# Performance work log

Hardware: AMD Instinct MI355X
Metric: run time of the kernel (lower is better)

## Reference

```python
import jax, jax.numpy as jnp
import numpy as np

MEAN_DEG = 3.8
QS = (2, 4, 8, 16, 32, 64)
POOL_DIM = 100
BP_ITERS = 10


def _bn(x, g, b):
    # BatchNorm1d in training mode: biased batch statistics over the node dim
    m = x.mean(0)
    v = ((x - m) ** 2).mean(0)
    return g * (x - m) * jax.lax.rsqrt(v + 1e-5) + b


def _gcn_sparse(x, src, dst, n, w, b):
    # GCNConv: add self loops, symmetric deg^-1/2 normalization, scatter-add aggregation
    loop = jnp.arange(n, dtype=src.dtype)
    s2 = jnp.concatenate([src, loop])
    d2 = jnp.concatenate([dst, loop])
    deg = jax.ops.segment_sum(jnp.ones(s2.shape[0], x.dtype), d2, num_segments=n)
    dinv = jnp.where(deg > 0, jax.lax.rsqrt(deg), 0.0)
    norm = (dinv[s2] * dinv[d2])[:, None]
    return jax.ops.segment_sum((x @ w)[s2] * norm, d2, num_segments=n) + b


def _gcn_dense(x, adj, w, b):
    # GCN on the dense pooled adjacency (pooled graphs are fully connected)
    n = adj.shape[-1]
    A = adj + jnp.eye(n, dtype=adj.dtype)
    d = A.sum(-1)
    dinv = jnp.where(d > 0, jax.lax.rsqrt(d), 0.0)
    An = dinv[:, :, None] * A * dinv[:, None, :]
    return jnp.einsum('bij,bjd->bid', An, x @ w) + b


def _bp(src, dst, n, q, beta, seed):
    # SBM-style belief propagation: iterate node marginals psi [n,q] for a fixed
    # number of sweeps; coupling exp(beta), global external field ~ mean_degree.
    key = jax.random.fold_in(jax.random.key(42), seed)
    psi0 = jax.nn.softmax(jax.random.normal(key, (n, q), jnp.float32), -1)
    eb = jnp.expm1(beta)

    def step(psi, _):
        msg = jax.ops.segment_sum(jnp.log1p(eb * psi[src]), dst, num_segments=n)
        field = (MEAN_DEG * beta / n) * psi.sum(0)
        return jax.nn.softmax(msg - field, -1), None

    psi, _ = jax.lax.scan(step, psi0, None, length=BP_ITERS)
    return psi


def _forward(x, w11, b11, g11, be11, w12, b12, g12, be12, w13, b13, g13, be13,
             bp_betas, pool_w, pool_b,
             w21, b21, g21, be21, w22, b22, g22, be22, w23, b23, g23, be23,
             fc1_w, fc1_b, fc2_w, fc2_b, edge_index, num_graphs):
    n = x.shape[0]
    B = num_graphs
    N = n // B
    src, dst = edge_index[0], edge_index[1]
    # per-graph dense adjacency (edge_index_to_csr -> todense, duplicates sum)
    adj = jnp.zeros((B, N, N), x.dtype).at[src // N, src % N, dst % N].add(1.0)

    # stage 1: three GCN + BN layers on the raw graph
    x11 = _bn(_gcn_sparse(x, src, dst, n, w11, b11), g11, be11)
    x12 = _bn(_gcn_sparse(x11, src, dst, n, w12, b12), g12, be12)
    x13 = _bn(_gcn_sparse(x12, src, dst, n, w13, b13), g13, be13)
    x1_out = jnp.concatenate([x11, x12, x13], -1).reshape(B, N, -1).max(1)  # [B,90]

    # six belief-propagation runs -> concat assignments [n, 2+4+...+64 = 126]
    s1 = jnp.concatenate([_bp(src, dst, n, q, bp_betas[i], i) for i, q in enumerate(QS)], -1)
    s1 = s1 @ pool_w + pool_b  # [n, 100]

    # dense diff-pool
    s1 = jax.nn.softmax(s1.reshape(B, N, POOL_DIM), -1)
    p1_x = jnp.einsum('bnk,bnd->bkd', s1, x13.reshape(B, N, -1))   # [B,100,30]
    p1_adj = jnp.einsum('bnk,bnm,bml->bkl', s1, adj, s1)           # [B,100,100]

    # stage 2: three dense GCN + BN layers on pooled graphs
    C = 30
    x21 = _bn(_gcn_dense(p1_x, p1_adj, w21, b21).reshape(-1, C), g21, be21)
    x22 = _bn(_gcn_dense(x21.reshape(B, POOL_DIM, C), p1_adj, w22, b22).reshape(-1, C), g22, be22)
    x23 = _bn(_gcn_dense(x22.reshape(B, POOL_DIM, C), p1_adj, w23, b23).reshape(-1, C), g23, be23)
    x2_out = jnp.concatenate([x21, x22, x23], -1).reshape(B, POOL_DIM, -1).max(1)  # [B,90]

    conv_out = jnp.concatenate([x1_out, x2_out], -1)  # [B,180]
    out = jax.nn.relu(conv_out @ fc1_w + fc1_b) @ fc2_w + fc2_b  # dropout p=0 -> identity
    return out, jnp.zeros((1,), x.dtype)


def setup_inputs() -> dict:
    key = jax.random.key(0)
    B, N, EP = 64, 1024, 8192
    ks = jax.random.split(key, 24)
    x = jax.random.normal(ks[0], (B * N, 3), jnp.float32)
    off = (jnp.arange(B, dtype=jnp.int32) * N)[:, None]
    src = (jax.random.randint(ks[1], (B, EP), 0, N, jnp.int32) + off).reshape(-1)
    dst = (jax.random.randint(ks[2], (B, EP), 0, N, jnp.int32) + off).reshape(-1)
    edge_index = jnp.stack([src, dst])

    def lin(k, i, o):
        return jax.random.normal(k, (i, o), jnp.float32) / np.sqrt(i)

    p = {}
    dims1 = [(3, 30), (30, 30), (30, 30)]
    for idx, (i, o) in enumerate(dims1, 1):
        p['w1%d' % idx] = lin(ks[2 + idx], i, o)
        p['b1%d' % idx] = jnp.zeros((o,), jnp.float32)
        p['g1%d' % idx] = jnp.ones((o,), jnp.float32)
        p['be1%d' % idx] = jnp.zeros((o,), jnp.float32)
    for idx in (1, 2, 3):
        p['w2%d' % idx] = lin(ks[8 + idx], 30, 30)
        p['b2%d' % idx] = jnp.zeros((30,), jnp.float32)
        p['g2%d' % idx] = jnp.ones((30,), jnp.float32)
        p['be2%d' % idx] = jnp.zeros((30,), jnp.float32)
    qs = np.array(QS, np.float32)
    p['bp_betas'] = jnp.asarray(np.log(qs / (np.sqrt(MEAN_DEG) - 1.0) + 1.0))
    p['pool_w'] = lin(ks[15], 126, 100); p['pool_b'] = jnp.zeros((100,), jnp.float32)
    p['fc1_w'] = lin(ks[16], 180, 50); p['fc1_b'] = jnp.zeros((50,), jnp.float32)
    p['fc2_w'] = lin(ks[17], 50, 6); p['fc2_b'] = jnp.zeros((6,), jnp.float32)
    return {'x': x, 'edge_index': edge_index, 'num_graphs': B, **p}


def reference(x, edge_index, num_graphs, w11, b11, g11, be11, w12, b12, g12, be12,
              w13, b13, g13, be13, bp_betas, pool_w, pool_b,
              w21, b21, g21, be21, w22, b22, g22, be22, w23, b23, g23, be23,
              fc1_w, fc1_b, fc2_w, fc2_b):
    return _forward(x, w11, b11, g11, be11, w12, b12, g12, be12, w13, b13, g13, be13,
                    bp_betas, pool_w, pool_b,
                    w21, b21, g21, be21, w22, b22, g22, be22, w23, b23, g23, be23,
                    fc1_w, fc1_b, fc2_w, fc2_b, edge_index, num_graphs)
```

## Files before the change

### kernel.cpp

```cpp
#include <hip/hip_runtime.h>
#include <stdint.h>
#include <float.h>


constexpr int NN    = 65536;
constexpr int NEDGE = 524288;
constexpr int NBG   = 64;

__constant__ int cQS[6]   = {2,4,8,16,32,64};

__device__ __forceinline__ void tf2x32(uint32_t k0, uint32_t k1, uint32_t x0, uint32_t x1,
                                       uint32_t& o0, uint32_t& o1){
  uint32_t ks[3] = {k0, k1, k0 ^ k1 ^ 0x1BD11BDAu};
  x0 += ks[0]; x1 += ks[1];
  const int RA[4] = {13,15,26,6}, RB[4] = {17,29,16,24};
  #pragma unroll
  for (int i=0;i<5;i++){
    const int* r = (i&1)? RB : RA;
    #pragma unroll
    for (int j=0;j<4;j++){
      x0 += x1;
      x1 = (x1 << r[j]) | (x1 >> (32 - r[j]));
      x1 ^= x0;
    }
    x0 += ks[(i+1)%3];
    x1 += ks[(i+2)%3] + (uint32_t)(i+1);
  }
  o0 = x0; o1 = x1;
}

__device__ __forceinline__ float erfinv32(float xx){
  #pragma clang fp contract(off)
  float w = -log1pf(-xx*xx);
  float p;
  if (w < 5.0f){
    w = w - 2.5f;
    p = 2.81022636e-08f;
    p = 3.43273939e-07f  + p*w;
    p = -3.5233877e-06f  + p*w;
    p = -4.39150654e-06f + p*w;
    p = 0.00021858087f   + p*w;
    p = -0.00125372503f  + p*w;
    p = -0.00417768164f  + p*w;
    p = 0.246640727f     + p*w;
    p = 1.50140941f      + p*w;
  } else {
    w = sqrtf(w) - 3.0f;
    p = -0.000200214257f;
    p = 0.000100950558f  + p*w;
    p = 0.00134934322f   + p*w;
    p = -0.00367342844f  + p*w;
    p = 0.00573950773f   + p*w;
    p = -0.0076224613f   + p*w;
    p = 0.00943887047f   + p*w;
    p = 1.00167406f      + p*w;
    p = 2.83297682f      + p*w;
  }
  return p*xx;
}

__global__ __launch_bounds__(256) void k_count(const int* __restrict__ src, const int* __restrict__ dst,
                                               int* __restrict__ degi, int* __restrict__ dego){
  int e = blockIdx.x*256 + threadIdx.x;
  if (e >= NEDGE) return;
  atomicAdd(&degi[dst[e]], 1);
  atomicAdd(&dego[src[e]], 1);
}

__global__ __launch_bounds__(256) void k_scan1(const int* __restrict__ degi, const int* __restrict__ dego,
                                               int* __restrict__ rpi, int* __restrict__ rpo,
                                               int* __restrict__ bsum){
  __shared__ int lds[256];
  const int* deg = blockIdx.y? dego : degi;
  int* rp = blockIdx.y? rpo : rpi;
  int* bs = bsum + blockIdx.y*256;
  int b = blockIdx.x, t = threadIdx.x;
  lds[t] = deg[b*256 + t];
  __syncthreads();
  for (int s=1;s<256;s<<=1){
    int add = (t>=s)? lds[t-s] : 0;
    __syncthreads();
    lds[t] += add;
    __syncthreads();
  }
  rp[b*256 + t + 1] = lds[t];
  if (t==0 && b==0) rp[0] = 0;
  if (t==255) bs[b] = lds[255];
}

__global__ __launch_bounds__(256) void k_scan2(int* __restrict__ bsum){
  __shared__ int lds[256];
  int* bs = bsum + blockIdx.x*256;
  int t = threadIdx.x;
  lds[t] = bs[t];
  __syncthreads();
  for (int s=1;s<256;s<<=1){
    int add = (t>=s)? lds[t-s] : 0;
    __syncthreads();
    lds[t] += add;
    __syncthreads();
  }
  bs[t] = (t==0)? 0 : lds[t-1];
}

__global__ __launch_bounds__(256) void k_scan3(int* __restrict__ rpi, int* __restrict__ rpo,
                                               const int* __restrict__ bsum){
  int* rp = blockIdx.y? rpo : rpi;
  const int* bs = bsum + blockIdx.y*256;
  int b = blockIdx.x, t = threadIdx.x;
  rp[b*256 + t + 1] += bs[b];
}

__global__ __launch_bounds__(256) void k_fill(const int* __restrict__ src, const int* __restrict__ dst,
                                              const int* __restrict__ rpi, const int* __restrict__ rpo,
                                              int* __restrict__ cntA, int* __restrict__ cntB,
                                              int* __restrict__ colI, int* __restrict__ colO){
  int e = blockIdx.x*256 + threadIdx.x;
  if (e >= NEDGE) return;
  if (blockIdx.y == 0){
    int d = dst[e];
    int p = atomicAdd(&cntA[d], 1);
    colI[rpi[d] + p] = e;
  } else {
    int d = src[e];
    int p = atomicAdd(&cntB[d], 1);
    colO[rpo[d] + p] = e;
  }
}

__global__ __launch_bounds__(256) void k_sortrow(const int* __restrict__ rpi, const int* __restrict__ rpo,
                                                 int* __restrict__ colI, int* __restrict__ colO,
                                                 const int* __restrict__ src, const int* __restrict__ dst){
  const int* rp = blockIdx.y? rpo : rpi;
  int* colbuf   = blockIdx.y? colO : colI;
  const int* other = blockIdx.y? dst : src;
  int v = blockIdx.x*256 + threadIdx.x;
  if (v >= NN) return;
  int s0 = rp[v], s1 = rp[v+1];
  for (int i=s0+1;i<s1;i++){
    int key = colbuf[i]; int j = i-1;
    while (j>=s0 && colbuf[j]>key){ colbuf[j+1]=colbuf[j]; j--; }
    colbuf[j+1] = key;
  }
  for (int i=s0;i<s1;i++) colbuf[i] = other[colbuf[i]];
}

__global__ __launch_bounds__(256) void k_dinv(const int* __restrict__ degi, float* __restrict__ dinv){
  int v = blockIdx.x*256 + threadIdx.x;
  if (v >= NN) return;
  dinv[v] = 1.0f / sqrtf((float)(degi[v] + 1));
}

template<int CIN>
__global__ __launch_bounds__(256) void k_mm30(const float* __restrict__ x, const float* __restrict__ w,
                                              float* __restrict__ h, int nrow){
  __shared__ float ws[CIN*30];
  int t = threadIdx.x;
  for (int i=t;i<CIN*30;i+=256) ws[i] = w[i];
  __syncthreads();
  int id = blockIdx.x*256 + t;
  if (id >= nrow*30) return;
  int v = id/30, j = id - v*30;
  const float* xr = x + v*CIN;
  float acc = 0.f;
  #pragma unroll
  for (int k=0;k<CIN;k++) acc += xr[k]*ws[k*30+j];
  h[id] = acc;
}

__global__ __launch_bounds__(256) void k_gcn_agg(const float* __restrict__ h, const int* __restrict__ rp,
    const int* __restrict__ col, const float* __restrict__ dinv, const float* __restrict__ bias,
    float* __restrict__ y){
  int b = blockIdx.x;
  int xcd = b & 7, i = b >> 3;
  int gs = i/60, j = i - gs*60;
  int graph = gs*8 + xcd;
  int idwg = j*256 + threadIdx.x;
  int rw = idwg/15, pr = idwg - rw*15;
  int v = graph*1024 + rw;
  float dv = dinv[v];
  float accx = 0.f, accy = 0.f;
  int a = rp[v], e = rp[v+1];
  for (; a+4<=e; a+=4){
    int s0=col[a], s1=col[a+1], s2=col[a+2], s3=col[a+3];
    float d0=dinv[s0], d1=dinv[s1], d2=dinv[s2], d3=dinv[s3];
    float2 h0=*(const float2*)(h+s0*30+2*pr), h1=*(const float2*)(h+s1*30+2*pr);
    float2 h2=*(const float2*)(h+s2*30+2*pr), h3=*(const float2*)(h+s3*30+2*pr);
    accx += h0.x*(d0*dv); accy += h0.y*(d0*dv);
    accx += h1.x*(d1*dv); accy += h1.y*(d1*dv);
    accx += h2.x*(d2*dv); accy += h2.y*(d2*dv);
    accx += h3.x*(d3*dv); accy += h3.y*(d3*dv);
  }
  for (; a<e; ++a){
    int s = col[a];
    float w = dinv[s]*dv;
    float2 hv = *(const float2*)(h+s*30+2*pr);
    accx += hv.x*w; accy += hv.y*w;
  }
  float2 hs = *(const float2*)(h + v*30 + 2*pr);
  float w2 = dv*dv;
  accx += hs.x*w2; accy += hs.y*w2;
  float2 o; o.x = accx + bias[2*pr]; o.y = accy + bias[2*pr+1];
  *(float2*)(y + v*30 + 2*pr) = o;
}

__global__ __launch_bounds__(256) void k_bn_stat(const float* __restrict__ x, int nrow,
    float* __restrict__ partS, float* __restrict__ partQ){
  __shared__ float lds[256*31];
  int b = blockIdx.x, t = threadIdx.x;
  int rows = nrow >> 8;
  float as[30], aq[30];
  #pragma unroll
  for (int f=0;f<30;f++){ as[f]=0.f; aq[f]=0.f; }
  for (int r=t; r<rows; r+=256){
    const float* xr = x + (b*rows + r)*30;
    #pragma unroll
    for (int f=0;f<30;f++){ float v = xr[f]; as[f] += v; aq[f] += v*v; }
  }
  #pragma unroll
  for (int f=0;f<30;f++) lds[t*31+f] = as[f];
  __syncthreads();
  for (int s=128;s>0;s>>=1){
    if (t<s){
      #pragma unroll
      for (int f=0;f<30;f++) lds[t*31+f] += lds[(t+s)*31+f];
    }
    __syncthreads();
  }
  if (t<30) partS[b*30+t] = lds[t];
  __syncthreads();
  #pragma unroll
  for (int f=0;f<30;f++) lds[t*31+f] = aq[f];
  __syncthreads();
  for (int s=128;s>0;s>>=1){
    if (t<s){
      #pragma unroll
      for (int f=0;f<30;f++) lds[t*31+f] += lds[(t+s)*31+f];
    }
    __syncthreads();
  }
  if (t<30) partQ[b*30+t] = lds[t];
}

__global__ void k_bn_red2(const float* __restrict__ partS, const float* __restrict__ partQ,
                          float n, float* __restrict__ mean, float* __restrict__ var){
  int f = threadIdx.x;
  if (f >= 30) return;
  float s = 0.f, q = 0.f;
  for (int b=0;b<256;b++){ s += partS[b*30+f]; q += partQ[b*30+f]; }
  float m = s / n;
  mean[f] = m;
  var[f]  = q / n - m*m;
}

__global__ __launch_bounds__(256) void k_bn_apply(const float* __restrict__ x, const float* __restrict__ mean,
    const float* __restrict__ var, const float* __restrict__ g, const float* __restrict__ be,
    float* __restrict__ out, int nrow){
  int id = blockIdx.x*256 + threadIdx.x;
  if (id >= nrow*30) return;
  int f = id % 30;
  out[id] = g[f]*(x[id]-mean[f]) * (1.0f/sqrtf(var[f]+1e-5f)) + be[f];
}

__device__ __forceinline__ void bp_decode2(int b, int& graph, int& run, int& jj){
  int xcd = b & 7, i = b >> 3;
  int gs = i >> 7, j = i & 127;
  if      (j <   4){ run=0; jj=j;    }
  else if (j <   8){ run=1; jj=j-4;  }
  else if (j <  16){ run=2; jj=j-8;  }
  else if (j <  32){ run=3; jj=j-16; }
  else if (j <  64){ run=4; jj=j-32; }
  else             { run=5; jj=j-64; }
  graph = gs*8 + xcd;
}

template<int TPR>
__device__ __forceinline__ void bfly_max4(float& m0, float& m1, float& m2, float& m3){
  if constexpr (TPR > 1){
    #pragma unroll
    for (int lm = TPR>>1; lm; lm >>= 1){
      float p0=__shfl_xor(m0,lm,64), p1=__shfl_xor(m1,lm,64);
      float p2=__shfl_xor(m2,lm,64), p3=__shfl_xor(m3,lm,64);
      m0=fmaxf(m0,p0); m1=fmaxf(m1,p1); m2=fmaxf(m2,p2); m3=fmaxf(m3,p3);
    }
  }
  { float t0=fmaxf(m0,m2), t1=fmaxf(m1,m3), t2=fmaxf(m2,m0), t3=fmaxf(m3,m1);
    m0=t0; m1=t1; m2=t2; m3=t3; }
  { float t0=fmaxf(m0,m1), t1=fmaxf(m1,m0), t2=fmaxf(m2,m3), t3=fmaxf(m3,m2);
    m0=t0; m1=t1; m2=t2; m3=t3; }
}

template<int TPR>
__device__ __forceinline__ void bfly_sum4(float& s0, float& s1, float& s2, float& s3){
  if constexpr (TPR > 1){
    #pragma unroll
    for (int lm = TPR>>1; lm; lm >>= 1){
      float p0=__shfl_xor(s0,lm,64), p1=__shfl_xor(s1,lm,64);
      float p2=__shfl_xor(s2,lm,64), p3=__shfl_xor(s3,lm,64);
      s0 += p0; s1 += p1; s2 += p2; s3 += p3;
    }
  }
  { float t0=s0+s2, t1=s1+s3, t2=s2+s0, t3=s3+s1;
    s0=t0; s1=t1; s2=t2; s3=t3; }
  { float t0=s0+s1, t1=s1+s0, t2=s2+s3, t3=s3+s2;
    s0=t0; s1=t1; s2=t2; s3=t3; }
}

template<int Q, int CO, int TPR, int L2T>
__device__ __forceinline__ void bp_first_elem2(int graph, int jj, float* __restrict__ psi_pk,
                                               float* __restrict__ lg, float eb,
                                               uint32_t k0, uint32_t k1){
  int idx = jj*256 + (int)threadIdx.x;
  if constexpr (Q == 2){
    int row = graph*1024 + idx;
    float z[2];
    #pragma unroll
    for (int r=0;r<2;r++){
      uint32_t b0,b1;
      tf2x32(k0,k1, 0u, (uint32_t)(row*2 + r), b0,b1);
      uint32_t bits = b0 ^ b1;
      float f = __uint_as_float((bits>>9) | 0x3F800000u) - 1.0f;
      const float lo = __uint_as_float(0xBF7FFFFFu);
      float u = fmaxf(lo, f*2.0f + lo);
      z[r] = __uint_as_float(0x3FB504F3u) * erfinv32(u);
    }
    float m0=fmaxf(z[0],z[1]), m1=fmaxf(z[1],z[0]);
    float e0=expf(z[0]-m0), e1=expf(z[1]-m1);
    float s0=e0+e1, s1=e1+e0;
    float p0=e0/s0, p1=e1/s1;
    ((float2*)(psi_pk + (size_t)NN*CO))[row] = make_float2(p0,p1);
    ((float2*)(lg     + (size_t)NN*CO))[row] = make_float2(log1pf(eb*p0), log1pf(eb*p1));
  } else {
    int rw = idx >> L2T, ct = idx & (TPR-1);
    int row = graph*1024 + rw;
    float z[4];
    #pragma unroll
    for (int r=0;r<4;r++){
      uint32_t b0,b1;
      tf2x32(k0,k1, 0u, (uint32_t)(row*Q + 4*ct + r), b0,b1);
      uint32_t bits = b0 ^ b1;
      float f = __uint_as_float((bits>>9) | 0x3F800000u) - 1.0f;
      const float lo = __uint_as_float(0xBF7FFFFFu);
      float u = fmaxf(lo, f*2.0f + lo);
      z[r] = __uint_as_float(0x3FB504F3u) * erfinv32(u);
    }
    float m0=z[0],m1=z[1],m2=z[2],m3=z[3];
    bfly_max4<TPR>(m0,m1,m2,m3);
    float e0=expf(z[0]-m0), e1=expf(z[1]-m1), e2=expf(z[2]-m2), e3=expf(z[3]-m3);
    float s0=e0,s1=e1,s2=e2,s3=e3;
    bfly_sum4<TPR>(s0,s1,s2,s3);
    float p0=e0/s0, p1=e1/s1, p2=e2/s2, p3=e3/s3;
    ((float4*)(psi_pk + (size_t)NN*CO))[(size_t)row*TPR + ct] = make_float4(p0,p1,p2,p3);
    ((float4*)(lg     + (size_t)NN*CO))[(size_t)row*TPR + ct] =
        make_float4(log1pf(eb*p0), log1pf(eb*p1), log1pf(eb*p2), log1pf(eb*p3));
  }
}

__global__ __launch_bounds__(256) void k_bp_first(float* __restrict__ psi_pk, float* __restrict__ lg,
                                                  const float* __restrict__ betas){
  int graph, run, jj;
  bp_decode2(blockIdx.x, graph, run, jj);
  uint32_t k0, k1;
  tf2x32(0u, 42u, 0u, (uint32_t)run, k0, k1);
  float eb = expm1f(betas[run]);
  switch(run){
    case 0: bp_first_elem2< 2, 0, 1,0>(graph, jj, psi_pk, lg, eb, k0, k1); break;
    case 1: bp_first_elem2< 4, 2, 1,0>(graph, jj, psi_pk, lg, eb, k0, k1); break;
    case 2: bp_first_elem2< 8, 6, 2,1>(graph, jj, psi_pk, lg, eb, k0, k1); break;
    case 3: bp_first_elem2<16,14, 4,2>(graph, jj, psi_pk, lg, eb, k0, k1); break;
    case 4: bp_first_elem2<32,30, 8,3>(graph, jj, psi_pk, lg, eb, k0, k1); break;
    default:bp_first_elem2<64,62,16,4>(graph, jj, psi_pk, lg, eb, k0, k1); break;
  }
}

template<int Q, int CO, int TPR, int L2T>
__device__ __forceinline__ void bp_step_elem2(int graph, int run, int jj,
    const float* __restrict__ lcur, float* __restrict__ nxt, float* __restrict__ lnxt,
    const int* __restrict__ rp, const int* __restrict__ col,
    const float* __restrict__ field, float eb, int fin){
  int idx = jj*256 + (int)threadIdx.x;
  if constexpr (Q == 2){
    int row = graph*1024 + idx;
    const float2* B2 = (const float2*)(lcur + (size_t)NN*CO);
    float a0=0.f, a1=0.f;
    int a = rp[row], b2 = rp[row+1];
    for (; a+8<=b2; a+=8){
      int s0=col[a],s1=col[a+1],s2=col[a+2],s3=col[a+3];
      int s4=col[a+4],s5=col[a+5],s6=col[a+6],s7=col[a+7];
      float2 u0=B2[s0], u1=B2[s1], u2=B2[s2], u3=B2[s3];
      float2 u4=B2[s4], u5=B2[s5], u6=B2[s6], u7=B2[s7];
      a0+=u0.x; a1+=u0.y; a0+=u1.x; a1+=u1.y;
      a0+=u2.x; a1+=u2.y; a0+=u3.x; a1+=u3.y;
      a0+=u4.x; a1+=u4.y; a0+=u5.x; a1+=u5.y;
      a0+=u6.x; a1+=u6.y; a0+=u7.x; a1+=u7.y;
    }
    for (; a+4<=b2; a+=4){
      int s0=col[a],s1=col[a+1],s2=col[a+2],s3=col[a+3];
      float2 u0=B2[s0], u1=B2[s1], u2=B2[s2], u3=B2[s3];
      a0+=u0.x; a1+=u0.y; a0+=u1.x; a1+=u1.y;
      a0+=u2.x; a1+=u2.y; a0+=u3.x; a1+=u3.y;
    }
    for (; a<b2; ++a){ float2 u=B2[col[a]]; a0+=u.x; a1+=u.y; }
    float v0 = a0 - field[run*64 + 0];
    float v1 = a1 - field[run*64 + 1];
    float m0=fmaxf(v0,v1), m1=fmaxf(v1,v0);
    float e0=expf(v0-m0), e1=expf(v1-m1);
    float s0=e0+e1, s1=e1+e0;
    float p0=e0/s0, p1=e1/s1;
    if (fin){
      float* o = nxt + (size_t)row*126 + CO;
      o[0]=p0; o[1]=p1;
    } else {
      ((float2*)(nxt  + (size_t)NN*CO))[row] = make_float2(p0,p1);
      ((float2*)(lnxt + (size_t)NN*CO))[row] = make_float2(log1pf(eb*p0), log1pf(eb*p1));
// ... 114 lines not shown

__global__ __launch_bounds__(256) void k_catT(const float* __restrict__ cat, float* __restrict__ catT){
  __shared__ float tile[64*127];
  int b = blockIdx.x, t = threadIdx.x;
  const float* src = cat + (size_t)b*64*126;
  for (int i=t;i<8064;i+=256){
    int r = i/126, k = i - r*126;
    tile[r*127 + k] = src[i];
  }
  __syncthreads();
  for (int i=t;i<8064;i+=256){
    int k = i>>6, r = i&63;
    catT[(size_t)k*65536 + b*64 + r] = tile[r*127 + k];
  }
}

__global__ __launch_bounds__(256) void k_s1t(const float* __restrict__ catT, const float* __restrict__ pw,
                                             const float* __restrict__ pb, float* __restrict__ s1){
  __shared__ float wl[12600];
  __shared__ float pbl[100];
  __shared__ float redM[2][128];
  __shared__ float redS[2][128];
  int t = threadIdx.x;
  for (int i=t;i<12600;i+=256) wl[i] = pw[i];
  if (t < 100) pbl[t] = pb[t];
  int w = t>>6, lane = t&63;
  int rh = w&1, chh = w>>1;
  int ch = chh*50;
  int row = blockIdx.x*128 + rh*64 + lane;
  __syncthreads();
  float acc[50];
  #pragma unroll
  for (int j=0;j<50;j++) acc[j] = pbl[ch+j];
  for (int k=0;k<126;k++){
    float xv = catT[(size_t)k*65536 + row];
    const float* wr = &wl[k*100 + ch];
    #pragma unroll
    for (int j=0;j<50;j+=2){
      float2 wv = *(const float2*)&wr[j];
      acc[j]   += xv*wv.x;
      acc[j+1] += xv*wv.y;
    }
  }
  float m = acc[0];
  #pragma unroll
  for (int j=1;j<50;j++) m = fmaxf(m, acc[j]);
  redM[chh][rh*64 + lane] = m;
  __syncthreads();
  float mm = fmaxf(redM[0][rh*64 + lane], redM[1][rh*64 + lane]);
  float s = 0.f;
  #pragma unroll
  for (int j=0;j<50;j++){ acc[j] = expf(acc[j]-mm); s += acc[j]; }
  redS[chh][rh*64 + lane] = s;
  __syncthreads();
  float tot = redS[0][rh*64 + lane] + redS[1][rh*64 + lane];
  float* o = s1 + (size_t)row*100 + ch;
  #pragma unroll
  for (int j=0;j<50;j+=2){
    float2 ov; ov.x = acc[j]/tot; ov.y = acc[j+1]/tot;
    *(float2*)&o[j] = ov;
  }
}

__global__ __launch_bounds__(256) void k_T(const float* __restrict__ s1, const int* __restrict__ rp,
                                           const int* __restrict__ col, float* __restrict__ T){
  int b = blockIdx.x;
  int xcd = b & 7, i = b >> 3;
  int gs = i/100, j = i - gs*100;
  int graph = gs*8 + xcd;
  int idwg = j*256 + threadIdx.x;
  int rw = idwg/25, quad = idwg - rw*25;
  int v = graph*1024 + rw;
  float a0=0.f,a1=0.f,a2=0.f,a3=0.f;
  const float4* S4 = (const float4*)s1;
  int a = rp[v], e = rp[v+1];
  for (; a+8<=e; a+=8){
    int s0=col[a], s1_=col[a+1], s2=col[a+2], s3=col[a+3];
    int s4=col[a+4], s5=col[a+5], s6=col[a+6], s7=col[a+7];
    float4 u0=S4[(size_t)s0*25+quad], u1=S4[(size_t)s1_*25+quad];
    float4 u2=S4[(size_t)s2*25+quad], u3=S4[(size_t)s3*25+quad];
    float4 u4=S4[(size_t)s4*25+quad], u5=S4[(size_t)s5*25+quad];
    float4 u6=S4[(size_t)s6*25+quad], u7=S4[(size_t)s7*25+quad];
    a0+=u0.x; a1+=u0.y; a2+=u0.z; a3+=u0.w;
    a0+=u1.x; a1+=u1.y; a2+=u1.z; a3+=u1.w;
    a0+=u2.x; a1+=u2.y; a2+=u2.z; a3+=u2.w;
    a0+=u3.x; a1+=u3.y; a2+=u3.z; a3+=u3.w;
    a0+=u4.x; a1+=u4.y; a2+=u4.z; a3+=u4.w;
    a0+=u5.x; a1+=u5.y; a2+=u5.z; a3+=u5.w;
    a0+=u6.x; a1+=u6.y; a2+=u6.z; a3+=u6.w;
    a0+=u7.x; a1+=u7.y; a2+=u7.z; a3+=u7.w;
  }
  for (; a+4<=e; a+=4){
    int s0=col[a], s1_=col[a+1], s2=col[a+2], s3=col[a+3];
    float4 u0=S4[(size_t)s0*25+quad], u1=S4[(size_t)s1_*25+quad];
    float4 u2=S4[(size_t)s2*25+quad], u3=S4[(size_t)s3*25+quad];
    a0+=u0.x; a1+=u0.y; a2+=u0.z; a3+=u0.w;
    a0+=u1.x; a1+=u1.y; a2+=u1.z; a3+=u1.w;
    a0+=u2.x; a1+=u2.y; a2+=u2.z; a3+=u2.w;
    a0+=u3.x; a1+=u3.y; a2+=u3.z; a3+=u3.w;
  }
  for (; a<e; ++a){
    float4 u = S4[(size_t)col[a]*25+quad];
    a0+=u.x; a1+=u.y; a2+=u.z; a3+=u.w;
  }
  ((float4*)T)[(size_t)v*25 + quad] = make_float4(a0,a1,a2,a3);
}

__global__ __launch_bounds__(512) void k_p1adj_sk(const float* __restrict__ s1, const float* __restrict__ T,
                                                  float* __restrict__ part){
  __shared__ float sS[6400];
  __shared__ float sT[6400];
  int blk = blockIdx.x;
  int b = blk >> 2, qtr = blk & 3;
  int t = threadIdx.x;
  int tk = t/20, tl = t - tk*20;
  bool act = t < 500;
  int k0 = tk*4, l0 = tl*5;
  float acc[4][5];
  #pragma unroll
  for (int i=0;i<4;i++)
    #pragma unroll
    for (int j=0;j<5;j++) acc[i][j] = 0.f;
  const float* s1b = s1 + (size_t)b*102400;
  const float* Tb  = T  + (size_t)b*102400;
  for (int c=qtr*4; c<qtr*4+4; c++){
    for (int i=t;i<6400;i+=512){ sS[i] = s1b[c*6400+i]; sT[i] = Tb[c*6400+i]; }
    __syncthreads();
    if (act){
      #pragma unroll 2
      for (int n=0;n<64;n++){
        const float* sr = &sS[n*100 + k0];
        const float* tr = &sT[n*100 + l0];
        float s0=sr[0], s1v=sr[1], s2=sr[2], s3=sr[3];
        float t0=tr[0], t1=tr[1], t2=tr[2], t3=tr[3], t4=tr[4];
        acc[0][0]+=s0*t0; acc[0][1]+=s0*t1; acc[0][2]+=s0*t2; acc[0][3]+=s0*t3; acc[0][4]+=s0*t4;
        acc[1][0]+=s1v*t0; acc[1][1]+=s1v*t1; acc[1][2]+=s1v*t2; acc[1][3]+=s1v*t3; acc[1][4]+=s1v*t4;
        acc[2][0]+=s2*t0; acc[2][1]+=s2*t1; acc[2][2]+=s2*t2; acc[2][3]+=s2*t3; acc[2][4]+=s2*t4;
        acc[3][0]+=s3*t0; acc[3][1]+=s3*t1; acc[3][2]+=s3*t2; acc[3][3]+=s3*t3; acc[3][4]+=s3*t4;
      }
    }
    __syncthreads();
  }
  if (act){
    float* pp = part + (size_t)qtr*640000 + (size_t)b*10000;
    #pragma unroll
    for (int i=0;i<4;i++){
      float* o = pp + (k0+i)*100 + l0;
      #pragma unroll
      for (int j=0;j<5;j++) o[j] = acc[i][j];
    }
  }
}

__global__ __launch_bounds__(256) void k_p1adj_red(const float* __restrict__ part, float* __restrict__ padj){
  int id = blockIdx.x*256 + threadIdx.x;
  if (id >= NBG*10000) return;
  float s = part[id];
  s += part[640000 + id];
  s += part[1280000 + id];
  s += part[1920000 + id];
  padj[id] = s;
}

__global__ __launch_bounds__(256) void k_p1x_sk(const float* __restrict__ s1, const float* __restrict__ x13,
                                                float* __restrict__ part){
  __shared__ float sS[6400];
  __shared__ float sX[1920];
  int blk = blockIdx.x;
  int b = blk >> 2, qtr = blk & 3;
  int t = threadIdx.x;
  int tk = t/10, tl = t - tk*10;
  bool act = t < 250;
  int k0 = tk*4, d0 = tl*3;
  float acc[4][3];
  #pragma unroll
  for (int i=0;i<4;i++)
    #pragma unroll
    for (int j=0;j<3;j++) acc[i][j] = 0.f;
  const float* s1b = s1 + (size_t)b*102400;
  const float* xb  = x13 + (size_t)b*30720;
  for (int c=qtr*4; c<qtr*4+4; c++){
    for (int i=t;i<6400;i+=256) sS[i] = s1b[c*6400+i];
    for (int i=t;i<1920;i+=256) sX[i] = xb[c*1920+i];
    __syncthreads();
    if (act){
      #pragma unroll 2
      for (int n=0;n<64;n++){
        const float* sr = &sS[n*100 + k0];
        const float* xr = &sX[n*30 + d0];
        float s0=sr[0], s1v=sr[1], s2=sr[2], s3=sr[3];
        float x0=xr[0], x1=xr[1], x2=xr[2];
        acc[0][0]+=s0*x0; acc[0][1]+=s0*x1; acc[0][2]+=s0*x2;
        acc[1][0]+=s1v*x0; acc[1][1]+=s1v*x1; acc[1][2]+=s1v*x2;
        acc[2][0]+=s2*x0; acc[2][1]+=s2*x1; acc[2][2]+=s2*x2;
        acc[3][0]+=s3*x0; acc[3][1]+=s3*x1; acc[3][2]+=s3*x2;
      }
    }
    __syncthreads();
  }
  if (act){
    float* pp = part + (size_t)qtr*192000 + (size_t)b*3000;
    #pragma unroll
    for (int i=0;i<4;i++){
      float* o = pp + (k0+i)*30 + d0;
      #pragma unroll
      for (int j=0;j<3;j++) o[j] = acc[i][j];
    }
  }
}

__global__ __launch_bounds__(256) void k_p1x_red(const float* __restrict__ part, float* __restrict__ px){
  int id = blockIdx.x*256 + threadIdx.x;
  if (id >= NBG*3000) return;
  float s = part[id];
  s += part[192000 + id];
  s += part[384000 + id];
  s += part[576000 + id];
  px[id] = s;
}

__global__ __launch_bounds__(256) void k_dinv2(const float* __restrict__ padj, float* __restrict__ dv){
  int id = blockIdx.x*256 + threadIdx.x;
  if (id >= NBG*100) return;
  const float* r = padj + id*100;
  int k = id % 100;
  float s = 0.f;
  for (int l=0;l<100;l++){
    float v = r[l];
    if (l==k) v += 1.0f;
    s += v;
  }
  dv[id] = 1.0f/sqrtf(s);
}

__global__ __launch_bounds__(256) void k_Ank(const float* __restrict__ padj, const float* __restrict__ dv,
                                             float* __restrict__ An){
  int id = blockIdx.x*256 + threadIdx.x;
  if (id >= NBG*10000) return;
  int b = id/10000;
  int rem = id - b*10000;
  int k = rem/100, l = rem - k*100;
  float a = padj[id] + ((k==l)? 1.0f : 0.0f);
  An[id] = (dv[b*100+k]*a)*dv[b*100+l];
}

__global__ __launch_bounds__(256) void k_y2(const float* __restrict__ An, const float* __restrict__ h,
    const float* __restrict__ bias, float* __restrict__ y){
  int id = blockIdx.x*256 + threadIdx.x;
  if (id >= NBG*100*30) return;
  int d = id % 30;
  int bk = id / 30;
  int b = bk / 100;
  const float* Ar = An + bk*100;
  const float* hb = h + b*100*30;
  float acc = 0.f;
  for (int l=0;l<100;l++) acc += Ar[l]*hb[l*30+d];
  y[id] = acc + bias[d];
}

__global__ __launch_bounds__(256) void k_pool2(const float* __restrict__ A,
    const float* __restrict__ Bv, const float* __restrict__ Cv,
    int rows, float* __restrict__ conv, int coff){
  __shared__ float lds[256*31];
  int b = blockIdx.x, a = blockIdx.y, t = threadIdx.x;
  const float* X = (a==0)? A : ((a==1)? Bv : Cv);
  float acc[30];
  #pragma unroll
  for (int f=0;f<30;f++) acc[f] = -FLT_MAX;
  for (int r=t; r<rows; r+=256){
    const float* xr = X + (size_t)(b*rows + r)*30;
    #pragma unroll
    for (int f=0;f<30;f++) acc[f] = fmaxf(acc[f], xr[f]);
  }
  #pragma unroll
  for (int f=0;f<30;f++) lds[t*31+f] = acc[f];
  __syncthreads();
  for (int s=128;s>0;s>>=1){
    if (t<s){
      #pragma unroll
      for (int f=0;f<30;f++) lds[t*31+f] = fmaxf(lds[t*31+f], lds[(t+s)*31+f]);
    }
    __syncthreads();
  }
  if (t<30) conv[b*180 + coff + a*30 + t] = lds[t];
}

__global__ __launch_bounds__(64) void k_fc(const float* __restrict__ conv,
    const float* __restrict__ w1, const float* __restrict__ b1,
    const float* __restrict__ w2, const float* __restrict__ b2, float* __restrict__ out){
  __shared__ float row[180];
  __shared__ float hid[50];
  int b = blockIdx.x, t = threadIdx.x;
  for (int i=t;i<180;i+=64) row[i] = conv[b*180+i];
  __syncthreads();
  if (t < 50){
    float a = b1[t];
    for (int i=0;i<180;i++) a += row[i]*w1[i*50+t];
    hid[t] = fmaxf(a, 0.f);
  }
  __syncthreads();
  if (t < 6){
    float a = b2[t];
    for (int i=0;i<50;i++) a += hid[i]*w2[i*6+t];
    out[b*6+t] = a;
  }
  if (b==0 && t==63) out[NBG*6] = 0.0f;
}

extern "C" void kernel_launch(void* const* d_in, const int* in_sizes, int n_in,
                              void* d_out, int out_size, void* d_ws, size_t ws_size,
                              hipStream_t stream)
{
  (void)in_sizes; (void)n_in; (void)out_size; (void)ws_size;
  const float* x   = (const float*)d_in[0];
  const int*   src = (const int*)d_in[1];
  const int*   dst = src + NEDGE;
  const float* w11=(const float*)d_in[3],  *b11=(const float*)d_in[4],  *g11=(const float*)d_in[5],  *be11=(const float*)d_in[6];
  const float* w12=(const float*)d_in[7],  *b12=(const float*)d_in[8],  *g12=(const float*)d_in[9],  *be12=(const float*)d_in[10];
  const float* w13=(const float*)d_in[11], *b13=(const float*)d_in[12], *g13=(const float*)d_in[13], *be13=(const float*)d_in[14];
  const float* w21=(const float*)d_in[15], *b21=(const float*)d_in[16], *g21=(const float*)d_in[17], *be21=(const float*)d_in[18];
  const float* w22=(const float*)d_in[19], *b22=(const float*)d_in[20], *g22=(const float*)d_in[21], *be22=(const float*)d_in[22];
  const float* w23=(const float*)d_in[23], *b23=(const float*)d_in[24], *g23=(const float*)d_in[25], *be23=(const float*)d_in[26];
  const float* betas=(const float*)d_in[27];
  const float* poolw=(const float*)d_in[28], *poolb=(const float*)d_in[29];
  const float* fc1w=(const float*)d_in[30], *fc1b=(const float*)d_in[31];
  const float* fc2w=(const float*)d_in[32], *fc2b=(const float*)d_in[33];
  float* out = (float*)d_out;

  uint8_t* basep = (uint8_t*)d_ws;
  size_t off = 0;
  auto take = [&](size_t bytes)->void*{
    void* p = basep + off;
    off = (off + bytes + 255) & ~(size_t)255;
    return p;
  };
  int* degi    = (int*)take((size_t)NN*4);
  int* dego    = (int*)take((size_t)NN*4);
  int* cntA    = (int*)take((size_t)NN*4);
  int* cntB    = (int*)take((size_t)NN*4);
  int* rp_in   = (int*)take((size_t)(NN+1)*4);
  int* rp_out  = (int*)take((size_t)(NN+1)*4);
  int* bsum    = (int*)take(512*4);
  int* col_in  = (int*)take((size_t)NEDGE*4);
  int* col_out = (int*)take((size_t)NEDGE*4);
  float* dinv  = (float*)take((size_t)NN*4);
  float* hbuf  = (float*)take((size_t)NN*30*4);
  float* tmpY  = (float*)take((size_t)NN*30*4);
  float* X1    = (float*)take((size_t)NN*30*4);
  float* X2    = (float*)take((size_t)NN*30*4);
  float* X3    = (float*)take((size_t)NN*30*4);
  float* bufA  = (float*)take((size_t)NN*126*4);
  float* bufB  = (float*)take((size_t)NN*126*4);
  float* logA  = (float*)take((size_t)NN*126*4);
  float* logB  = (float*)take((size_t)NN*126*4);
  float* partCS= (float*)take((size_t)6*256*64*4);
  float* fieldv= (float*)take(384*4);
  float* partBN= (float*)take(256*30*4);
  float* partBN2=(float*)take(256*30*4);
  float* meanv = (float*)take(128);
  float* varv  = (float*)take(128);
  float* px    = (float*)take(192000*4);
  float* padj  = (float*)take(640000*4);
  float* An    = (float*)take(640000*4);
  float* dinv2 = (float*)take(6400*4);
  float* h2    = (float*)take(192000*4);
  float* y2    = (float*)take(192000*4);
  float* X21   = (float*)take(192000*4);
  float* X22   = (float*)take(192000*4);
  float* X23   = (float*)take(192000*4);
  float* conv  = (float*)take(64*180*4);

  float* catT     = logA;
  float* pAdjPart = logB;
  float* pPxPart  = logB + 2560000;

  hipMemsetAsync(degi, 0, (size_t)4*NN*4, stream);
  k_count<<<2048,256,0,stream>>>(src,dst,degi,dego);
  k_scan1<<<dim3(256,2),256,0,stream>>>(degi, dego, rp_in, rp_out, bsum);
  k_scan2<<<2,256,0,stream>>>(bsum);
  k_scan3<<<dim3(256,2),256,0,stream>>>(rp_in, rp_out, bsum);
  k_fill<<<dim3(2048,2),256,0,stream>>>(src, dst, rp_in, rp_out, cntA, cntB, col_in, col_out);
  k_sortrow<<<dim3(256,2),256,0,stream>>>(rp_in, rp_out, col_in, col_out, src, dst);
  k_dinv<<<256,256,0,stream>>>(degi, dinv);

  auto run_bn = [&](const float* yin, float* xout, const float* g, const float* be, int nrow){
    k_bn_stat<<<256,256,0,stream>>>(yin, nrow, partBN, partBN2);
    k_bn_red2<<<1,32,0,stream>>>(partBN, partBN2, (float)nrow, meanv, varv);
    k_bn_apply<<<(nrow*30)/256,256,0,stream>>>(yin, meanv, varv, g, be, xout, nrow);
  };

  k_mm30<3><<<7680,256,0,stream>>>(x, w11, hbuf, NN);
  k_gcn_agg<<<3840,256,0,stream>>>(hbuf, rp_in, col_in, dinv, b11, tmpY);
  run_bn(tmpY, X1, g11, be11, NN);
  k_mm30<30><<<7680,256,0,stream>>>(X1, w12, hbuf, NN);
  k_gcn_agg<<<3840,256,0,stream>>>(hbuf, rp_in, col_in, dinv, b12, tmpY);
  run_bn(tmpY, X2, g12, be12, NN);
  k_mm30<30><<<7680,256,0,stream>>>(X2, w13, hbuf, NN);
  k_gcn_agg<<<3840,256,0,stream>>>(hbuf, rp_in, col_in, dinv, b13, tmpY);
  run_bn(tmpY, X3, g13, be13, NN);
  k_pool2<<<dim3(NBG,3),256,0,stream>>>(X1, X2, X3, 1024, conv, 0);

  k_bp_first<<<8192,256,0,stream>>>(bufA, logA, betas);
  float* cur = bufA;  float* nxt = bufB;
  float* lcur = logA; float* lnxt = logB;
  for (int it=0; it<10; ++it){
    k_colsum_part<<<1536,64,0,stream>>>(cur, partCS);
    k_field<<<1,384,0,stream>>>(partCS, betas, fieldv);
    int fin = (it==9);
    k_bp_step<<<8192,256,0,stream>>>(nxt, lcur, lnxt, rp_in, col_in, fieldv, betas, fin);
    float* tp = cur;  cur = nxt;   nxt = tp;
    float* tl = lcur; lcur = lnxt; lnxt = tl;
  }

  k_catT<<<1024,256,0,stream>>>(bufA, catT);
  k_s1t<<<512,256,0,stream>>>(catT, poolw, poolb, bufB);
  k_T<<<6400,256,0,stream>>>(bufB, rp_out, col_out, bufA);
  k_p1adj_sk<<<256,512,0,stream>>>(bufB, bufA, pAdjPart);
  k_p1adj_red<<<2500,256,0,stream>>>(pAdjPart, padj);
  k_p1x_sk<<<256,256,0,stream>>>(bufB, X3, pPxPart);
  k_p1x_red<<<750,256,0,stream>>>(pPxPart, px);
  k_dinv2<<<25,256,0,stream>>>(padj, dinv2);
  k_Ank<<<2500,256,0,stream>>>(padj, dinv2, An);

  auto gcn2 = [&](const float* xin, const float* w, const float* bb, const float* g,
                  const float* be, float* xout){
    k_mm30<30><<<750,256,0,stream>>>(xin, w, h2, NBG*100);
    k_y2<<<750,256,0,stream>>>(An, h2, bb, y2);
    run_bn(y2, xout, g, be, NBG*100);
  };
  gcn2(px,  w21, b21, g21, be21, X21);
  gcn2(X21, w22, b22, g22, be22, X22);
  gcn2(X22, w23, b23, g23, be23, X23);
  k_pool2<<<dim3(NBG,3),256,0,stream>>>(X21, X22, X23, 100, conv, 90);

  k_fc<<<64,64,0,stream>>>(conv, fc1w, fc1b, fc2w, fc2b, out);
}
```

Baseline: 1.345 ms.

## Fold BatchNorm into next layer weights and fuse BN statistics into aggregation

BatchNorm statistics are now accumulated with LDS and global atomics inside the GCN aggregation and dense y2 kernels. A single small kernel turns them into a per-feature scale and shift and folds those into the next layer's weight matrix and bias. Elsewhere the affine is applied on the fly in pooling and in the pooled-feature load, so the separate stat, reduce and apply passes and their intermediate buffers go away. It also merges dinv into the row sort, combines the two partial reductions, and fuses the pooled-graph degree and normalisation step into one kernel. In exchange it adds atomic contention on 64 slots and uses a one-pass variance formula (E[x²]−m², as before) with atomic ordering nondeterminism.

```diff
diff --git a/kernel.cpp b/kernel.cpp
--- a/kernel.cpp
+++ b/kernel.cpp
@@ -130,7 +130,8 @@
 
 __global__ __launch_bounds__(256) void k_sortrow(const int* __restrict__ rpi, const int* __restrict__ rpo,
                                                  int* __restrict__ colI, int* __restrict__ colO,
-                                                 const int* __restrict__ src, const int* __restrict__ dst){
+                                                 const int* __restrict__ src, const int* __restrict__ dst,
+                                                 const int* __restrict__ degi, float* __restrict__ dinv){
   const int* rp = blockIdx.y? rpo : rpi;
   int* colbuf   = blockIdx.y? colO : colI;
   const int* other = blockIdx.y? dst : src;
@@ -143,12 +144,7 @@
     colbuf[j+1] = key;
   }
   for (int i=s0;i<s1;i++) colbuf[i] = other[colbuf[i]];
-}
-
-__global__ __launch_bounds__(256) void k_dinv(const int* __restrict__ degi, float* __restrict__ dinv){
-  int v = blockIdx.x*256 + threadIdx.x;
-  if (v >= NN) return;
-  dinv[v] = 1.0f / sqrtf((float)(degi[v] + 1));
+  if (blockIdx.y == 0) dinv[v] = 1.0f / sqrtf((float)(degi[v] + 1));
 }
 
 template<int CIN>
@@ -168,14 +164,36 @@
   h[id] = acc;
 }
 
+__global__ __launch_bounds__(256) void k_mm30c(const float* __restrict__ x, const float* __restrict__ wfold,
+                                               const float* __restrict__ cvec, float* __restrict__ h, int nrow){
+  __shared__ float ws[900];
+  __shared__ float cl[30];
+  int t = threadIdx.x;
+  for (int i=t;i<900;i+=256) ws[i] = wfold[i];
+  if (t < 30) cl[t] = cvec[t];
+  __syncthreads();
+  int id = blockIdx.x*256 + t;
+  if (id >= nrow*30) return;
+  int v = id/30, j = id - v*30;
+  const float* xr = x + v*30;
+  float acc = cl[j];
+  #pragma unroll
+  for (int k=0;k<30;k++) acc += xr[k]*ws[k*30+j];
+  h[id] = acc;
+}
+
 __global__ __launch_bounds__(256) void k_gcn_agg(const float* __restrict__ h, const int* __restrict__ rp,
     const int* __restrict__ col, const float* __restrict__ dinv, const float* __restrict__ bias,
-    float* __restrict__ y){
+    float* __restrict__ y, float* __restrict__ gS, float* __restrict__ gQ){
+  __shared__ float binS[30], binQ[30];
+  int t = threadIdx.x;
+  if (t < 30){ binS[t]=0.f; binQ[t]=0.f; }
+  __syncthreads();
   int b = blockIdx.x;
   int xcd = b & 7, i = b >> 3;
   int gs = i/60, j = i - gs*60;
   int graph = gs*8 + xcd;
-  int idwg = j*256 + threadIdx.x;
+  int idwg = j*256 + t;
   int rw = idwg/15, pr = idwg - rw*15;
   int v = graph*1024 + rw;
   float dv = dinv[v];
@@ -202,64 +220,43 @@
   accx += hs.x*w2; accy += hs.y*w2;
   float2 o; o.x = accx + bias[2*pr]; o.y = accy + bias[2*pr+1];
   *(float2*)(y + v*30 + 2*pr) = o;
-}
-
-__global__ __launch_bounds__(256) void k_bn_stat(const float* __restrict__ x, int nrow,
-    float* __restrict__ partS, float* __restrict__ partQ){
-  __shared__ float lds[256*31];
-  int b = blockIdx.x, t = threadIdx.x;
-  int rows = nrow >> 8;
-  float as[30], aq[30];
-  #pragma unroll
-  for (int f=0;f<30;f++){ as[f]=0.f; aq[f]=0.f; }
-  for (int r=t; r<rows; r+=256){
-    const float* xr = x + (b*rows + r)*30;
-    #pragma unroll
-    for (int f=0;f<30;f++){ float v = xr[f]; as[f] += v; aq[f] += v*v; }
-  }
-  #pragma unroll
-  for (int f=0;f<30;f++) lds[t*31+f] = as[f];
-  __syncthreads();
-  for (int s=128;s>0;s>>=1){
-    if (t<s){
-      #pragma unroll
-      for (int f=0;f<30;f++) lds[t*31+f] += lds[(t+s)*31+f];
-    }
-    __syncthreads();
-  }
-  if (t<30) partS[b*30+t] = lds[t];
-  __syncthreads();
-  #pragma unroll
-  for (int f=0;f<30;f++) lds[t*31+f] = aq[f];
-  __syncthreads();
-  for (int s=128;s>0;s>>=1){
-    if (t<s){
-      #pragma unroll
-      for (int f=0;f<30;f++) lds[t*31+f] += lds[(t+s)*31+f];
-    }
-    __syncthreads();
-  }
-  if (t<30) partQ[b*30+t] = lds[t];
-}
-
-__global__ void k_bn_red2(const float* __restrict__ partS, const float* __restrict__ partQ,
-                          float n, float* __restrict__ mean, float* __restrict__ var){
-  int f = threadIdx.x;
-  if (f >= 30) return;
-  float s = 0.f, q = 0.f;
-  for (int b=0;b<256;b++){ s += partS[b*30+f]; q += partQ[b*30+f]; }
-  float m = s / n;
-  mean[f] = m;
-  var[f]  = q / n - m*m;
-}
-
-__global__ __launch_bounds__(256) void k_bn_apply(const float* __restrict__ x, const float* __restrict__ mean,
-    const float* __restrict__ var, const float* __restrict__ g, const float* __restrict__ be,
-    float* __restrict__ out, int nrow){
-  int id = blockIdx.x*256 + threadIdx.x;
-  if (id >= nrow*30) return;
-  int f = id % 30;
-  out[id] = g[f]*(x[id]-mean[f]) * (1.0f/sqrtf(var[f]+1e-5f)) + be[f];
+  atomicAdd(&binS[2*pr],   o.x); atomicAdd(&binQ[2*pr],   o.x*o.x);
+  atomicAdd(&binS[2*pr+1], o.y); atomicAdd(&binQ[2*pr+1], o.y*o.y);
+  __syncthreads();
+  if (t < 30){
+    int slot = (b & 63)*30 + t;
+    atomicAdd(&gS[slot], binS[t]);
+    atomicAdd(&gQ[slot], binQ[t]);
+  }
+}
+
+template<int FOLD>
+__global__ __launch_bounds__(256) void k_bnw(float* __restrict__ gS, float* __restrict__ gQ, float n,
+    const float* __restrict__ g, const float* __restrict__ be,
+    const float* __restrict__ wnext, float* __restrict__ sfc,
+    float* __restrict__ wfold, float* __restrict__ cvec){
+  __shared__ float s_l[30], c_l[30];
+  int t = threadIdx.x;
+  if (t < 30){
+    float s=0.f, q=0.f;
+    for (int u=0;u<64;u++){ s += gS[u*30+t]; q += gQ[u*30+t]; }
+    float m = s/n;
+    float var = q/n - m*m;
+    float sc = g[t]*(1.0f/sqrtf(var+1e-5f));
+    float c0 = be[t] - sc*m;
+    s_l[t]=sc; c_l[t]=c0;
+    sfc[t]=sc; sfc[32+t]=c0;
+    for (int u=0;u<64;u++){ gS[u*30+t]=0.f; gQ[u*30+t]=0.f; }
+  }
+  __syncthreads();
+  if (FOLD){
+    for (int i=t;i<900;i+=256) wfold[i] = s_l[i/30]*wnext[i];
+    if (t<30){
+      float c=0.f;
+      for (int k=0;k<30;k++) c += c_l[k]*wnext[k*30+t];
+      cvec[t]=c;
+    }
+  }
 }
 
 __device__ __forceinline__ void bp_decode2(int b, int& graph, int& run, int& jj){
@@ -680,18 +677,8 @@
   }
 }
 
-__global__ __launch_bounds__(256) void k_p1adj_red(const float* __restrict__ part, float* __restrict__ padj){
-  int id = blockIdx.x*256 + threadIdx.x;
-  if (id >= NBG*10000) return;
-  float s = part[id];
-  s += part[640000 + id];
-  s += part[1280000 + id];
-  s += part[1920000 + id];
-  padj[id] = s;
-}
-
-__global__ __launch_bounds__(256) void k_p1x_sk(const float* __restrict__ s1, const float* __restrict__ x13,
-                                                float* __restrict__ part){
+__global__ __launch_bounds__(256) void k_p1x_sk(const float* __restrict__ s1, const float* __restrict__ y3,
+                                                const float* __restrict__ sfc, float* __restrict__ part){
   __shared__ float sS[6400];
   __shared__ float sX[1920];
   int blk = blockIdx.x;
@@ -706,10 +693,13 @@
     #pragma unroll
     for (int j=0;j<3;j++) acc[i][j] = 0.f;
   const float* s1b = s1 + (size_t)b*102400;
-  const float* xb  = x13 + (size_t)b*30720;
+  const float* xb  = y3 + (size_t)b*30720;
   for (int c=qtr*4; c<qtr*4+4; c++){
     for (int i=t;i<6400;i+=256) sS[i] = s1b[c*6400+i];
-    for (int i=t;i<1920;i+=256) sX[i] = xb[c*1920+i];
+    for (int i=t;i<1920;i+=256){
+      int f = i % 30;
+      sX[i] = sfc[f]*xb[c*1920+i] + sfc[32+f];
+    }
     __syncthreads();
     if (act){
       #pragma unroll 2
@@ -737,68 +727,86 @@
   }
 }
 
-__global__ __launch_bounds__(256) void k_p1x_red(const float* __restrict__ part, float* __restrict__ px){
+__global__ __launch_bounds__(256) void k_ppred(const float* __restrict__ partA, const float* __restrict__ partX,
+                                               float* __restrict__ padj, float* __restrict__ px){
   int id = blockIdx.x*256 + threadIdx.x;
-  if (id >= NBG*3000) return;
-  float s = part[id];
-  s += part[192000 + id];
-  s += part[384000 + id];
-  s += part[576000 + id];
-  px[id] = s;
-}
-
-__global__ __launch_bounds__(256) void k_dinv2(const float* __restrict__ padj, float* __restrict__ dv){
-  int id = blockIdx.x*256 + threadIdx.x;
-  if (id >= NBG*100) return;
-  const float* r = padj + id*100;
-  int k = id % 100;
-  float s = 0.f;
-  for (int l=0;l<100;l++){
-    float v = r[l];
-    if (l==k) v += 1.0f;
-    s += v;
-  }
-  dv[id] = 1.0f/sqrtf(s);
-}
-
-__global__ __launch_bounds__(256) void k_Ank(const float* __restrict__ padj, const float* __restrict__ dv,
-                                             float* __restrict__ An){
-  int id = blockIdx.x*256 + threadIdx.x;
-  if (id >= NBG*10000) return;
-  int b = id/10000;
-  int rem = id - b*10000;
-  int k = rem/100, l = rem - k*100;
-  float a = padj[id] + ((k==l)? 1.0f : 0.0f);
-  An[id] = (dv[b*100+k]*a)*dv[b*100+l];
+  if (id < 640000){
+    float s = partA[id] + partA[640000+id] + partA[1280000+id] + partA[1920000+id];
+    padj[id] = s;
+  } else if (id < 832000){
+    int j = id - 640000;
+    float s = partX[j] + partX[192000+j] + partX[384000+j] + partX[576000+j];
+    px[j] = s;
+  }
+}
+
+__global__ __launch_bounds__(256) void k_An1(const float* __restrict__ padj, float* __restrict__ An){
+  __shared__ float dv[100];
+  int b = blockIdx.x, t = threadIdx.x;
+  if (t < 100){
+    const float* r = padj + (size_t)b*10000 + t*100;
+    float s = 0.f;
+    for (int l=0;l<100;l++){
+      float v = r[l];
+      if (l==t) v += 1.0f;
+      s += v;
+    }
+    dv[t] = 1.0f/sqrtf(s);
+  }
+  __syncthreads();
+  for (int i=t;i<10000;i+=256){
+    int k = i/100, l = i - k*100;
+    float a = padj[(size_t)b*10000 + i] + ((k==l)? 1.0f : 0.0f);
+    An[(size_t)b*10000 + i] = (dv[k]*a)*dv[l];
+  }
 }
 
 __global__ __launch_bounds__(256) void k_y2(const float* __restrict__ An, const float* __restrict__ h,
-    const float* __restrict__ bias, float* __restrict__ y){
-  int id = blockIdx.x*256 + threadIdx.x;
-  if (id >= NBG*100*30) return;
-  int d = id % 30;
-  int bk = id / 30;
-  int b = bk / 100;
-  const float* Ar = An + bk*100;
-  const float* hb = h + b*100*30;
-  float acc = 0.f;
-  for (int l=0;l<100;l++) acc += Ar[l]*hb[l*30+d];
-  y[id] = acc + bias[d];
+    const float* __restrict__ bias, float* __restrict__ y,
+    float* __restrict__ gS, float* __restrict__ gQ){
+  __shared__ float binS[30], binQ[30];
+  int t = threadIdx.x;
+  if (t < 30){ binS[t]=0.f; binQ[t]=0.f; }
+  __syncthreads();
+  int id = blockIdx.x*256 + t;
+  float val = 0.f;
+  int d = 0;
+  if (id < NBG*100*30){
+    d = id % 30;
+    int bk = id / 30;
+    int b = bk / 100;
+    const float* Ar = An + bk*100;
+    const float* hb = h + b*100*30;
+    float acc = 0.f;
+    for (int l=0;l<100;l++) acc += Ar[l]*hb[l*30+d];
+    val = acc + bias[d];
+    y[id] = val;
+    atomicAdd(&binS[d], val);
+    atomicAdd(&binQ[d], val*val);
+  }
+  __syncthreads();
+  if (t < 30){
+    int slot = (blockIdx.x & 63)*30 + t;
+    atomicAdd(&gS[slot], binS[t]);
+    atomicAdd(&gQ[slot], binQ[t]);
+  }
 }
 
 __global__ __launch_bounds__(256) void k_pool2(const float* __restrict__ A,
     const float* __restrict__ Bv, const float* __restrict__ Cv,
+    const float* __restrict__ sfcBase,
     int rows, float* __restrict__ conv, int coff){
   __shared__ float lds[256*31];
   int b = blockIdx.x, a = blockIdx.y, t = threadIdx.x;
   const float* X = (a==0)? A : ((a==1)? Bv : Cv);
+  const float* sf = sfcBase + a*64;
   float acc[30];
   #pragma unroll
   for (int f=0;f<30;f++) acc[f] = -FLT_MAX;
   for (int r=t; r<rows; r+=256){
     const float* xr = X + (size_t)(b*rows + r)*30;
     #pragma unroll
-    for (int f=0;f<30;f++) acc[f] = fmaxf(acc[f], xr[f]);
+    for (int f=0;f<30;f++) acc[f] = fmaxf(acc[f], sf[f]*xr[f] + sf[32+f]);
   }
   #pragma unroll
   for (int f=0;f<30;f++) lds[t*31+f] = acc[f];
@@ -866,6 +874,8 @@
   int* dego    = (int*)take((size_t)NN*4);
   int* cntA    = (int*)take((size_t)NN*4);
   int* cntB    = (int*)take((size_t)NN*4);
+  float* gS    = (float*)take(64*30*4);
+  float* gQ    = (float*)take(64*30*4);
   int* rp_in   = (int*)take((size_t)(NN+1)*4);
   int* rp_out  = (int*)take((size_t)(NN+1)*4);
   int* bsum    = (int*)take(512*4);
@@ -873,7 +883,6 @@
   int* col_out = (int*)take((size_t)NEDGE*4);
   float* dinv  = (float*)take((size_t)NN*4);
   float* hbuf  = (float*)take((size_t)NN*30*4);
-  float* tmpY  = (float*)take((size_t)NN*30*4);
   float* X1    = (float*)take((size_t)NN*30*4);
   float* X2    = (float*)take((size_t)NN*30*4);
   float* X3    = (float*)take((size_t)NN*30*4);
@@ -883,16 +892,13 @@
   float* logB  = (float*)take((size_t)NN*126*4);
   float* partCS= (float*)take((size_t)6*256*64*4);
   float* fieldv= (float*)take(384*4);
-  float* partBN= (float*)take(256*30*4);
-  float* partBN2=(float*)take(256*30*4);
-  float* meanv = (float*)take(128);
-  float* varv  = (float*)take(128);
+  float* sfcAll= (float*)take(6*64*4);
+  float* wfold = (float*)take(960*4);
+  float* cvec  = (float*)take(32*4);
   float* px    = (float*)take(192000*4);
   float* padj  = (float*)take(640000*4);
   float* An    = (float*)take(640000*4);
-  float* dinv2 = (float*)take(6400*4);
   float* h2    = (float*)take(192000*4);
-  float* y2    = (float*)take(192000*4);
   float* X21   = (float*)take(192000*4);
   float* X22   = (float*)take(192000*4);
   float* X23   = (float*)take(192000*4);
@@ -902,31 +908,24 @@
   float* pAdjPart = logB;
   float* pPxPart  = logB + 2560000;
 
-  hipMemsetAsync(degi, 0, (size_t)4*NN*4, stream);
+  hipMemsetAsync(degi, 0, (size_t)4*NN*4 + 2*64*30*4, stream);
   k_count<<<2048,256,0,stream>>>(src,dst,degi,dego);
   k_scan1<<<dim3(256,2),256,0,stream>>>(degi, dego, rp_in, rp_out, bsum);
   k_scan2<<<2,256,0,stream>>>(bsum);
   k_scan3<<<dim3(256,2),256,0,stream>>>(rp_in, rp_out, bsum);
   k_fill<<<dim3(2048,2),256,0,stream>>>(src, dst, rp_in, rp_out, cntA, cntB, col_in, col_out);
-  k_sortrow<<<dim3(256,2),256,0,stream>>>(rp_in, rp_out, col_in, col_out, src, dst);
-  k_dinv<<<256,256,0,stream>>>(degi, dinv);
-
-  auto run_bn = [&](const float* yin, float* xout, const float* g, const float* be, int nrow){
-    k_bn_stat<<<256,256,0,stream>>>(yin, nrow, partBN, partBN2);
-    k_bn_red2<<<1,32,0,stream>>>(partBN, partBN2, (float)nrow, meanv, varv);
-    k_bn_apply<<<(nrow*30)/256,256,0,stream>>>(yin, meanv, varv, g, be, xout, nrow);
-  };
+  k_sortrow<<<dim3(256,2),256,0,stream>>>(rp_in, rp_out, col_in, col_out, src, dst, degi, dinv);
 
   k_mm30<3><<<7680,256,0,stream>>>(x, w11, hbuf, NN);
-  k_gcn_agg<<<3840,256,0,stream>>>(hbuf, rp_in, col_in, dinv, b11, tmpY);
-  run_bn(tmpY, X1, g11, be11, NN);
-  k_mm30<30><<<7680,256,0,stream>>>(X1, w12, hbuf, NN);
-  k_gcn_agg<<<3840,256,0,stream>>>(hbuf, rp_in, col_in, dinv, b12, tmpY);
-  run_bn(tmpY, X2, g12, be12, NN);
-  k_mm30<30><<<7680,256,0,stream>>>(X2, w13, hbuf, NN);
-  k_gcn_agg<<<3840,256,0,stream>>>(hbuf, rp_in, col_in, dinv, b13, tmpY);
-  run_bn(tmpY, X3, g13, be13, NN);
-  k_pool2<<<dim3(NBG,3),256,0,stream>>>(X1, X2, X3, 1024, conv, 0);
+  k_gcn_agg<<<3840,256,0,stream>>>(hbuf, rp_in, col_in, dinv, b11, X1, gS, gQ);
+  k_bnw<1><<<1,256,0,stream>>>(gS, gQ, 65536.f, g11, be11, w12, sfcAll+0*64, wfold, cvec);
+  k_mm30c<<<7680,256,0,stream>>>(X1, wfold, cvec, hbuf, NN);
+  k_gcn_agg<<<3840,256,0,stream>>>(hbuf, rp_in, col_in, dinv, b12, X2, gS, gQ);
+  k_bnw<1><<<1,256,0,stream>>>(gS, gQ, 65536.f, g12, be12, w13, sfcAll+1*64, wfold, cvec);
+  k_mm30c<<<7680,256,0,stream>>>(X2, wfold, cvec, hbuf, NN);
+  k_gcn_agg<<<3840,256,0,stream>>>(hbuf, rp_in, col_in, dinv, b13, X3, gS, gQ);
+  k_bnw<0><<<1,256,0,stream>>>(gS, gQ, 65536.f, g13, be13, nullptr, sfcAll+2*64, nullptr, nullptr);
+  k_pool2<<<dim3(NBG,3),256,0,stream>>>(X1, X2, X3, sfcAll, 1024, conv, 0);
 
   k_bp_first<<<8192,256,0,stream>>>(bufA, logA, betas);
   float* cur = bufA;  float* nxt = bufB;
@@ -944,22 +943,20 @@
   k_s1t<<<512,256,0,stream>>>(catT, poolw, poolb, bufB);
   k_T<<<6400,256,0,stream>>>(bufB, rp_out, col_out, bufA);
   k_p1adj_sk<<<256,512,0,stream>>>(bufB, bufA, pAdjPart);
-  k_p1adj_red<<<2500,256,0,stream>>>(pAdjPart, padj);
-  k_p1x_sk<<<256,256,0,stream>>>(bufB, X3, pPxPart);
-  k_p1x_red<<<750,256,0,stream>>>(pPxPart, px);
-  k_dinv2<<<25,256,0,stream>>>(padj, dinv2);
-  k_Ank<<<2500,256,0,stream>>>(padj, dinv2, An);
-
-  auto gcn2 = [&](const float* xin, const float* w, const float* bb, const float* g,
-                  const float* be, float* xout){
-    k_mm30<30><<<750,256,0,stream>>>(xin, w, h2, NBG*100);
-    k_y2<<<750,256,0,stream>>>(An, h2, bb, y2);
-    run_bn(y2, xout, g, be, NBG*100);
-  };
-  gcn2(px,  w21, b21, g21, be21, X21);
-  gcn2(X21, w22, b22, g22, be22, X22);
-  gcn2(X22, w23, b23, g23, be23, X23);
-  k_pool2<<<dim3(NBG,3),256,0,stream>>>(X21, X22, X23, 100, conv, 90);
+  k_p1x_sk<<<256,256,0,stream>>>(bufB, X3, sfcAll+2*64, pPxPart);
+  k_ppred<<<3250,256,0,stream>>>(pAdjPart, pPxPart, padj, px);
+  k_An1<<<64,256,0,stream>>>(padj, An);
+
+  k_mm30<30><<<750,256,0,stream>>>(px, w21, h2, NBG*100);
+  k_y2<<<750,256,0,stream>>>(An, h2, b21, X21, gS, gQ);
+  k_bnw<1><<<1,256,0,stream>>>(gS, gQ, 6400.f, g21, be21, w22, sfcAll+3*64, wfold, cvec);
+  k_mm30c<<<750,256,0,stream>>>(X21, wfold, cvec, h2, NBG*100);
+  k_y2<<<750,256,0,stream>>>(An, h2, b22, X22, gS, gQ);
+  k_bnw<1><<<1,256,0,stream>>>(gS, gQ, 6400.f, g22, be22, w23, sfcAll+4*64, wfold, cvec);
+  k_mm30c<<<750,256,0,stream>>>(X22, wfold, cvec, h2, NBG*100);
+  k_y2<<<750,256,0,stream>>>(An, h2, b23, X23, gS, gQ);
+  k_bnw<0><<<1,256,0,stream>>>(gS, gQ, 6400.f, g23, be23, nullptr, sfcAll+5*64, nullptr, nullptr);
+  k_pool2<<<dim3(NBG,3),256,0,stream>>>(X21, X22, X23, sfcAll+3*64, 100, conv, 90);
 
   k_fc<<<64,64,0,stream>>>(conv, fc1w, fc1b, fc2w, fc2b, out);
 }
```

New measurement: 1.288 ms. -4.3%, faster.
